# Kernel optimization log

Hardware: AMD Instinct MI355X
Metric: run time of the kernel (lower is better)

The kernel has to match this reference:

```python
import jax, jax.numpy as jnp
import numpy as np

B, S, T = 64, 512, 32
H2 = 1024          # hidden_size * 2
ATT = 512          # attention_size


def setup_inputs() -> dict:
    key = jax.random.key(0)
    k1, k2, k3, k4, k5, k6 = jax.random.split(key, 6)
    h = jax.random.normal(k1, (B, S, H2), dtype=jnp.float32)
    h_mask = jax.random.randint(k2, (B, S), 0, 2).astype(jnp.int32)
    ht = jax.random.normal(k3, (B, T, H2), dtype=jnp.float32)
    # Linear params (xavier-ish scale)
    w1_w = jax.random.normal(k4, (ATT, 2 * H2), dtype=jnp.float32) * (1.0 / np.sqrt(2 * H2))
    w1_b = jax.random.normal(k5, (ATT,), dtype=jnp.float32) * 0.02
    u_w = jax.random.normal(k6, (1, ATT), dtype=jnp.float32) * (1.0 / np.sqrt(ATT))
    return {"h": h, "h_mask": h_mask, "ht": ht, "w1_w": w1_w, "w1_b": w1_b, "u_w": u_w}


def reference(h, h_mask, ht, w1_w, w1_b, u_w):
    # h: [B,S,2H], ht: [B,T,2H], h_mask: [B,S] (1 = valid, 0 = pad)
    valid = h_mask != 0                                  # [B,S]
    ht_mean = jnp.mean(ht, axis=1, keepdims=True)        # [B,1,2H]
    h_cat = jnp.concatenate(
        [h, jnp.broadcast_to(ht_mean, h.shape)], axis=2)  # [B,S,4H]
    h_cat = jnp.where(valid[..., None], h_cat, 0.0)
    a = jnp.tanh(jnp.einsum('bsf,af->bsa', h_cat, w1_w) + w1_b)  # [B,S,ATT]
    a = jnp.where(valid[..., None], a, 0.0)
    beta = jnp.einsum('bsa,a->bs', a, u_w[0])            # [B,S]
    beta = jnp.where(valid, beta, -1e20)
    alpha = jax.nn.softmax(beta, axis=1)                 # [B,S]
    s = jnp.einsum('bs,bsd->bd', alpha, h)               # [B,2H]
    return s
```

## Files before the change

### kernel.cpp

```cpp
#include <hip/hip_runtime.h>
#include <math.h>
#include <stdint.h>

#define Bb 64
#define Ss 512
#define Tt 32
#define H2 1024
#define FF 2048
#define ATT 512
#define MM (Bb * Ss)

typedef short bf8 __attribute__((ext_vector_type(8)));
typedef float f4 __attribute__((ext_vector_type(4)));

__device__ __forceinline__ unsigned short f2bf(float f) {
    unsigned u = __float_as_uint(f);
    u = (u + 0x7fffu + ((u >> 16) & 1u)) >> 16;
    return (unsigned short)u;
}

__device__ __forceinline__ void gl_lds16(const void* g, void* l) {
    __builtin_amdgcn_global_load_lds((const __attribute__((address_space(1))) void*)g,
                                     (__attribute__((address_space(3))) void*)l, 16, 0, 0);
}

__global__ void init_kernel(float* __restrict__ beta, float* __restrict__ out) {
    int i = blockIdx.x * 256 + threadIdx.x;
    if (i < Bb * Ss) beta[i] = 0.0f;
    if (i < Bb * H2) out[i] = 0.0f;
}

__global__ void mean_kernel(const float* __restrict__ ht, float* __restrict__ ht_mean) {
    int b = blockIdx.x;
    int d4 = threadIdx.x;
    const float4* p = (const float4*)(ht + (size_t)b * Tt * H2);
    float4 acc = make_float4(0.f, 0.f, 0.f, 0.f);
    #pragma unroll 4
    for (int t = 0; t < Tt; ++t) {
        float4 v = p[(size_t)t * (H2 / 4) + d4];
        acc.x += v.x; acc.y += v.y; acc.z += v.z; acc.w += v.w;
    }
    const float inv = 1.0f / (float)Tt;
    acc.x *= inv; acc.y *= inv; acc.z *= inv; acc.w *= inv;
    ((float4*)(ht_mean + (size_t)b * H2))[d4] = acc;
}

__global__ __launch_bounds__(256) void c2_kernel2(const float* __restrict__ ht_mean,
                                                  const float* __restrict__ w1_w,
                                                  const float* __restrict__ w1_b,
                                                  float* __restrict__ c2) {
    __shared__ float hm[H2];
    int b = blockIdx.x;
    for (int i = threadIdx.x; i < H2; i += 256) hm[i] = ht_mean[(size_t)b * H2 + i];
    __syncthreads();
    int a = blockIdx.y * 64 + ((int)threadIdx.x >> 2);
    int q = (int)threadIdx.x & 3;
    const float4* w   = (const float4*)(w1_w + (size_t)a * FF + H2 + q * 256);
    const float4* hm4 = (const float4*)(hm + q * 256);
    float acc = 0.f;
    #pragma unroll 8
    for (int k = 0; k < 64; ++k) {
        float4 wv = w[k]; float4 hv = hm4[k];
        acc += wv.x * hv.x + wv.y * hv.y + wv.z * hv.z + wv.w * hv.w;
    }
    acc += __shfl_xor(acc, 1);
    acc += __shfl_xor(acc, 2);
    if (q == 0) c2[(size_t)b * ATT + a] = acc + w1_b[a];
}

__global__ void convh_kernel(const float* __restrict__ in, unsigned short* __restrict__ out) {
    size_t i = ((size_t)blockIdx.x * 256 + threadIdx.x) * 8;
    float4 a = *(const float4*)(in + i);
    float4 b = *(const float4*)(in + i + 4);
    bf8 v = { (short)f2bf(a.x), (short)f2bf(a.y), (short)f2bf(a.z), (short)f2bf(a.w),
              (short)f2bf(b.x), (short)f2bf(b.y), (short)f2bf(b.z), (short)f2bf(b.w) };
    *(bf8*)(out + i) = v;
}

__global__ void convw_kernel(const float* __restrict__ w1_w, unsigned short* __restrict__ out) {
    size_t e = ((size_t)blockIdx.x * 256 + threadIdx.x) * 8;
    int row = (int)(e >> 10);
    int c = (int)(e & 1023);
    const float* src = w1_w + (size_t)row * FF + c;
    float4 a = *(const float4*)(src);
    float4 b = *(const float4*)(src + 4);
    bf8 v = { (short)f2bf(a.x), (short)f2bf(a.y), (short)f2bf(a.z), (short)f2bf(a.w),
              (short)f2bf(b.x), (short)f2bf(b.y), (short)f2bf(b.z), (short)f2bf(b.w) };
    *(bf8*)(out + e) = v;
}

__global__ __launch_bounds__(256) void gemm_mfma_kernel(
        const unsigned short* __restrict__ hb, const unsigned short* __restrict__ wb,
        const float* __restrict__ c2, const float* __restrict__ u_w,
        float* __restrict__ beta) {
    __shared__ __align__(16) unsigned short As[128][32];
    __shared__ __align__(16) unsigned short Bs[128][32];

    const int tid = (int)threadIdx.x;
    const int m0 = blockIdx.x * 128;
    const int n0 = blockIdx.y * 128;
    const int wid = tid >> 6, lane = tid & 63;
    const int wr = (wid >> 1) * 64;
    const int wc = (wid & 1) * 64;
    const int col = lane & 15, rg = lane >> 4;

    f4 acc[4][4] = {};

    const int srow = tid >> 2;
    const int skq = (tid & 3) * 8;
    const unsigned short* a0 = hb + (size_t)(m0 + srow) * H2 + skq;
    const unsigned short* b0 = wb + (size_t)(n0 + srow) * H2 + skq;
    unsigned short* lA = &As[0][0] + (size_t)wid * 512;
    unsigned short* lB = &Bs[0][0] + (size_t)wid * 512;

    for (int k0 = 0; k0 < H2; k0 += 32) {
        gl_lds16(a0 + k0, lA);
        gl_lds16(a0 + k0 + (size_t)64 * H2, lA + 2048);
        gl_lds16(b0 + k0, lB);
        gl_lds16(b0 + k0 + (size_t)64 * H2, lB + 2048);
        __syncthreads();
        bf8 av[4], bv[4];
        #pragma unroll
        for (int i = 0; i < 4; ++i) {
            av[i] = *(const bf8*)&As[wr + i * 16 + col][rg * 8];
            bv[i] = *(const bf8*)&Bs[wc + i * 16 + col][rg * 8];
        }
        #pragma unroll
        for (int i = 0; i < 4; ++i)
            #pragma unroll
            for (int j = 0; j < 4; ++j)
                acc[i][j] = __builtin_amdgcn_mfma_f32_16x16x32_bf16(av[i], bv[j], acc[i][j], 0, 0, 0);
        __syncthreads();
    }

    const int b_idx = blockIdx.x >> 2;
    const float* c2b = c2 + (size_t)b_idx * ATT + n0 + wc;
    const float* ub = u_w + n0 + wc;
    #pragma unroll
    for (int i = 0; i < 4; ++i) {
        float rp[4] = {0.f, 0.f, 0.f, 0.f};
        #pragma unroll
        for (int j = 0; j < 4; ++j) {
            int n = j * 16 + col;
            float cv = c2b[n];
            float uv = ub[n];
            #pragma unroll
            for (int r = 0; r < 4; ++r)
                rp[r] += tanhf(acc[i][j][r] + cv) * uv;
        }
        #pragma unroll
        for (int r = 0; r < 4; ++r) {
            float v = rp[r];
            v += __shfl_xor(v, 1);
            v += __shfl_xor(v, 2);
            v += __shfl_xor(v, 4);
            v += __shfl_xor(v, 8);
            if (col == 0)
                atomicAdd(&beta[(size_t)m0 + wr + i * 16 + rg * 4 + r], v);
        }
    }
}

__global__ __launch_bounds__(256) void gemm_beta_kernel(
        const float* __restrict__ h, const float* __restrict__ w1_w,
        const float* __restrict__ c2, const float* __restrict__ u_w,
        float* __restrict__ beta) {
    __shared__ float As[32][128];
    __shared__ float Bs[32][128];
    const int m0 = blockIdx.x * 128;
    const int n0 = blockIdx.y * 128;
    const int tid = (int)threadIdx.x;
    const int lrow = tid & 31;
    const int kq = tid >> 5;
    const int tx = tid & 15;
    const int ty = tid >> 4;
    float acc[8][8] = {};
    const float* Ag = h + (size_t)(m0 + lrow) * H2 + kq * 4;
    const float* Bg = w1_w + (size_t)(n0 + lrow) * FF + kq * 4;
    for (int k0 = 0; k0 < H2; k0 += 32) {
        #pragma unroll
        for (int p = 0; p < 4; ++p) {
            float4 av = *(const float4*)(Ag + (size_t)(p * 32) * H2 + k0);
            float4 bv = *(const float4*)(Bg + (size_t)(p * 32) * FF + k0);
            int r = lrow + p * 32;
            int kk = kq * 4;
            As[kk + 0][r] = av.x; As[kk + 1][r] = av.y; As[kk + 2][r] = av.z; As[kk + 3][r] = av.w;
            Bs[kk + 0][r] = bv.x; Bs[kk + 1][r] = bv.y; Bs[kk + 2][r] = bv.z; Bs[kk + 3][r] = bv.w;
        }
        __syncthreads();
        #pragma unroll
        for (int k = 0; k < 32; ++k) {
            float4 a0 = *(const float4*)&As[k][ty * 8];
            float4 a1 = *(const float4*)&As[k][ty * 8 + 4];
            float4 b0 = *(const float4*)&Bs[k][tx * 8];
            float4 b1 = *(const float4*)&Bs[k][tx * 8 + 4];
            float av[8] = {a0.x, a0.y, a0.z, a0.w, a1.x, a1.y, a1.z, a1.w};
            float bv[8] = {b0.x, b0.y, b0.z, b0.w, b1.x, b1.y, b1.z, b1.w};
            #pragma unroll
            for (int i = 0; i < 8; ++i)
                #pragma unroll
                for (int j = 0; j < 8; ++j)
                    acc[i][j] = fmaf(av[i], bv[j], acc[i][j]);
        }
        __syncthreads();
    }
    const int b_idx = m0 / Ss;
    float rowp[8] = {};
    #pragma unroll
    for (int j = 0; j < 8; ++j) {
        int n = n0 + tx * 8 + j;
        float c2v = c2[(size_t)b_idx * ATT + n];
        float uv = u_w[n];
        #pragma unroll
        for (int i = 0; i < 8; ++i)
            rowp[i] = fmaf(tanhf(acc[i][j] + c2v), uv, rowp[i]);
    }
    #pragma unroll
    for (int i = 0; i < 8; ++i) {
        float v = rowp[i];
        v += __shfl_xor(v, 8, 16);
        v += __shfl_xor(v, 4, 16);
        v += __shfl_xor(v, 2, 16);
        v += __shfl_xor(v, 1, 16);
        if (tx == 0) atomicAdd(&beta[(size_t)m0 + ty * 8 + i], v);
    }
}

__global__ void softmax_kernel(const float* __restrict__ beta, const int* __restrict__ h_mask,
                               float* __restrict__ alpha) {
    __shared__ float red[16];
    int b = blockIdx.x;
    int s = (int)threadIdx.x;
    float v = (h_mask[(size_t)b * Ss + s] != 0) ? beta[(size_t)b * Ss + s] : -1e20f;
    float m = v;
    #pragma unroll
    for (int off = 32; off >= 1; off >>= 1) m = fmaxf(m, __shfl_xor(m, off, 64));
    int wave = s >> 6;
    if ((s & 63) == 0) red[wave] = m;
    __syncthreads();
    float mx = red[0];
    #pragma unroll
    for (int w = 1; w < 8; ++w) mx = fmaxf(mx, red[w]);
    float e = expf(v - mx);
    float sum = e;
    #pragma unroll
    for (int off = 32; off >= 1; off >>= 1) sum += __shfl_xor(sum, off, 64);
    __syncthreads();
    if ((s & 63) == 0) red[8 + wave] = sum;
    __syncthreads();
    float tot = 0.f;
    #pragma unroll
    for (int w = 0; w < 8; ++w) tot += red[8 + w];
    alpha[(size_t)b * Ss + s] = e / tot;
}

__global__ void wsum_kernel(const float* __restrict__ h, const float* __restrict__ alpha,
                            float* __restrict__ out) {
    int b = blockIdx.x;
    int d = blockIdx.y * 256 + (int)threadIdx.x;
    int s0 = blockIdx.z * 128;
    const float* hp = h + (size_t)b * Ss * H2 + (size_t)s0 * H2 + d;
    const float* ap = alpha + (size_t)b * Ss + s0;
    float acc = 0.f;
    #pragma unroll 4
    for (int s = 0; s < 128; ++s) acc = fmaf(ap[s], hp[(size_t)s * H2], acc);
    atomicAdd(&out[(size_t)b * H2 + d], acc);
}

extern "C" void kernel_launch(void* const* d_in, const int* in_sizes, int n_in,
                              void* d_out, int out_size, void* d_ws, size_t ws_size,
                              hipStream_t stream) {
    const float* h      = (const float*)d_in[0];
    const int*   h_mask = (const int*)d_in[1];
    const float* ht     = (const float*)d_in[2];
    const float* w1_w   = (const float*)d_in[3];
    const float* w1_b   = (const float*)d_in[4];
    const float* u_w    = (const float*)d_in[5];
    float* out = (float*)d_out;

    float* ws      = (float*)d_ws;
    float* ht_mean = ws;
    float* c2      = ws + 65536;
    float* beta    = ws + 98304;
    float* alpha   = ws + 131072;
    unsigned short* w1a_bf = (unsigned short*)((char*)d_ws + 659456);
    unsigned short* h_bf   = (unsigned short*)((char*)d_ws + 659456 + 1048576);
    const size_t need = 659456 + 1048576 + (size_t)MM * H2 * 2;

    hipLaunchKernelGGL(init_kernel, dim3(256), dim3(256), 0, stream, beta, out);
    hipLaunchKernelGGL(mean_kernel, dim3(Bb), dim3(256), 0, stream, ht, ht_mean);
    hipLaunchKernelGGL(c2_kernel2, dim3(Bb, 8), dim3(256), 0, stream, ht_mean, w1_w, w1_b, c2);

    if (ws_size >= need) {
        hipLaunchKernelGGL(convw_kernel, dim3(256), dim3(256), 0, stream, w1_w, w1a_bf);
        hipLaunchKernelGGL(convh_kernel, dim3(16384), dim3(256), 0, stream, h, h_bf);
        hipLaunchKernelGGL(gemm_mfma_kernel, dim3(MM / 128, ATT / 128), dim3(256), 0, stream,
                           h_bf, w1a_bf, c2, u_w, beta);
    } else {
        hipLaunchKernelGGL(gemm_beta_kernel, dim3(MM / 128, ATT / 128), dim3(256), 0, stream,
                           h, w1_w, c2, u_w, beta);
    }

    hipLaunchKernelGGL(softmax_kernel, dim3(Bb), dim3(512), 0, stream, beta, h_mask, alpha);
    hipLaunchKernelGGL(wsum_kernel, dim3(Bb, H2 / 256, 4), dim3(256), 0, stream, h, alpha, out);
}
```

Baseline: 323.2 us.

## Fuse h bf16 conversion into GEMM with full-N tiles and drop beta atomics

Removes the separate h-to-bf16 conversion pass by loading fp32 h directly in the GEMM and converting it in registers before storing to LDS. The tile changes to 64 rows by the full 512 attention columns, so each block computes complete beta rows and reduces across waves in shared memory instead of using atomics. This also removes the beta zero-init. It cuts roughly 200MB of intermediate bf16 traffic, but h loads are now plain synchronous global loads with no async LDS path, and the weight tile is re-read by 512 blocks.

```diff
diff --git a/kernel.cpp b/kernel.cpp
--- a/kernel.cpp
+++ b/kernel.cpp
@@ -10,7 +10,12 @@
 #define ATT 512
 #define MM (Bb * Ss)
 
+#define BM 64
+#define BN 512
+#define BK 32
+
 typedef short bf8 __attribute__((ext_vector_type(8)));
+typedef short bf4 __attribute__((ext_vector_type(4)));
 typedef float f4 __attribute__((ext_vector_type(4)));
 
 __device__ __forceinline__ unsigned short f2bf(float f) {
@@ -24,10 +29,9 @@
                                      (__attribute__((address_space(3))) void*)l, 16, 0, 0);
 }
 
-__global__ void init_kernel(float* __restrict__ beta, float* __restrict__ out) {
+__global__ void init_kernel(float* __restrict__ out) {
     int i = blockIdx.x * 256 + threadIdx.x;
-    if (i < Bb * Ss) beta[i] = 0.0f;
-    if (i < Bb * H2) out[i] = 0.0f;
+    out[i] = 0.0f;
 }
 
 __global__ void mean_kernel(const float* __restrict__ ht, float* __restrict__ ht_mean) {
@@ -66,15 +70,6 @@
     acc += __shfl_xor(acc, 1);
     acc += __shfl_xor(acc, 2);
     if (q == 0) c2[(size_t)b * ATT + a] = acc + w1_b[a];
-}
-
-__global__ void convh_kernel(const float* __restrict__ in, unsigned short* __restrict__ out) {
-    size_t i = ((size_t)blockIdx.x * 256 + threadIdx.x) * 8;
-    float4 a = *(const float4*)(in + i);
-    float4 b = *(const float4*)(in + i + 4);
-    bf8 v = { (short)f2bf(a.x), (short)f2bf(a.y), (short)f2bf(a.z), (short)f2bf(a.w),
-              (short)f2bf(b.x), (short)f2bf(b.y), (short)f2bf(b.z), (short)f2bf(b.w) };
-    *(bf8*)(out + i) = v;
 }
 
 __global__ void convw_kernel(const float* __restrict__ w1_w, unsigned short* __restrict__ out) {
@@ -89,41 +84,41 @@
     *(bf8*)(out + e) = v;
 }
 
-__global__ __launch_bounds__(256) void gemm_mfma_kernel(
-        const unsigned short* __restrict__ hb, const unsigned short* __restrict__ wb,
+__global__ __launch_bounds__(512) void gemm_fused_kernel(
+        const float* __restrict__ h, const unsigned short* __restrict__ wb,
         const float* __restrict__ c2, const float* __restrict__ u_w,
         float* __restrict__ beta) {
-    __shared__ __align__(16) unsigned short As[128][32];
-    __shared__ __align__(16) unsigned short Bs[128][32];
+    __shared__ __align__(16) unsigned short As[BM][BK];
+    __shared__ __align__(16) unsigned short Bs[BN][BK];
+    __shared__ float red[8][64];
 
     const int tid = (int)threadIdx.x;
-    const int m0 = blockIdx.x * 128;
-    const int n0 = blockIdx.y * 128;
+    const int m0 = blockIdx.x * BM;
     const int wid = tid >> 6, lane = tid & 63;
-    const int wr = (wid >> 1) * 64;
-    const int wc = (wid & 1) * 64;
     const int col = lane & 15, rg = lane >> 4;
 
     f4 acc[4][4] = {};
 
-    const int srow = tid >> 2;
-    const int skq = (tid & 3) * 8;
-    const unsigned short* a0 = hb + (size_t)(m0 + srow) * H2 + skq;
-    const unsigned short* b0 = wb + (size_t)(n0 + srow) * H2 + skq;
-    unsigned short* lA = &As[0][0] + (size_t)wid * 512;
+    const int arow = tid >> 3;
+    const int aq   = (tid & 7) * 4;
+    const float* Ag = h + (size_t)(m0 + arow) * H2 + aq;
+    const int brow = tid >> 2;
+    const int bq   = (tid & 3) * 8;
     unsigned short* lB = &Bs[0][0] + (size_t)wid * 512;
 
-    for (int k0 = 0; k0 < H2; k0 += 32) {
-        gl_lds16(a0 + k0, lA);
-        gl_lds16(a0 + k0 + (size_t)64 * H2, lA + 2048);
-        gl_lds16(b0 + k0, lB);
-        gl_lds16(b0 + k0 + (size_t)64 * H2, lB + 2048);
+    for (int k0 = 0; k0 < H2; k0 += BK) {
+        #pragma unroll
+        for (int c = 0; c < 4; ++c)
+            gl_lds16(wb + (size_t)(c * 128 + brow) * H2 + k0 + bq, lB + c * 4096);
+        float4 a4 = *(const float4*)(Ag + k0);
+        bf4 ab = { (short)f2bf(a4.x), (short)f2bf(a4.y), (short)f2bf(a4.z), (short)f2bf(a4.w) };
+        *(bf4*)&As[arow][aq] = ab;
         __syncthreads();
         bf8 av[4], bv[4];
         #pragma unroll
         for (int i = 0; i < 4; ++i) {
-            av[i] = *(const bf8*)&As[wr + i * 16 + col][rg * 8];
-            bv[i] = *(const bf8*)&Bs[wc + i * 16 + col][rg * 8];
+            av[i] = *(const bf8*)&As[i * 16 + col][rg * 8];
+            bv[i] = *(const bf8*)&Bs[wid * 64 + i * 16 + col][rg * 8];
         }
         #pragma unroll
         for (int i = 0; i < 4; ++i)
@@ -133,96 +128,38 @@
         __syncthreads();
     }
 
-    const int b_idx = blockIdx.x >> 2;
-    const float* c2b = c2 + (size_t)b_idx * ATT + n0 + wc;
-    const float* ub = u_w + n0 + wc;
-    #pragma unroll
-    for (int i = 0; i < 4; ++i) {
-        float rp[4] = {0.f, 0.f, 0.f, 0.f};
-        #pragma unroll
-        for (int j = 0; j < 4; ++j) {
-            int n = j * 16 + col;
-            float cv = c2b[n];
-            float uv = ub[n];
+    const int b_idx = blockIdx.x >> 3;
+    const float* c2b = c2 + (size_t)b_idx * ATT + wid * 64;
+    const float* ub  = u_w + wid * 64;
+    float rp[4][4] = {};
+    #pragma unroll
+    for (int j = 0; j < 4; ++j) {
+        int n = j * 16 + col;
+        float cv = c2b[n];
+        float uv = ub[n];
+        #pragma unroll
+        for (int i = 0; i < 4; ++i)
             #pragma unroll
             for (int r = 0; r < 4; ++r)
-                rp[r] += tanhf(acc[i][j][r] + cv) * uv;
-        }
+                rp[i][r] += tanhf(acc[i][j][r] + cv) * uv;
+    }
+    #pragma unroll
+    for (int i = 0; i < 4; ++i)
         #pragma unroll
         for (int r = 0; r < 4; ++r) {
-            float v = rp[r];
+            float v = rp[i][r];
             v += __shfl_xor(v, 1);
             v += __shfl_xor(v, 2);
             v += __shfl_xor(v, 4);
             v += __shfl_xor(v, 8);
-            if (col == 0)
-                atomicAdd(&beta[(size_t)m0 + wr + i * 16 + rg * 4 + r], v);
+            if (col == 0) red[wid][i * 16 + rg * 4 + r] = v;
         }
-    }
-}
-
-__global__ __launch_bounds__(256) void gemm_beta_kernel(
-        const float* __restrict__ h, const float* __restrict__ w1_w,
-        const float* __restrict__ c2, const float* __restrict__ u_w,
-        float* __restrict__ beta) {
-    __shared__ float As[32][128];
-    __shared__ float Bs[32][128];
-    const int m0 = blockIdx.x * 128;
-    const int n0 = blockIdx.y * 128;
-    const int tid = (int)threadIdx.x;
-    const int lrow = tid & 31;
-    const int kq = tid >> 5;
-    const int tx = tid & 15;
-    const int ty = tid >> 4;
-    float acc[8][8] = {};
-    const float* Ag = h + (size_t)(m0 + lrow) * H2 + kq * 4;
-    const float* Bg = w1_w + (size_t)(n0 + lrow) * FF + kq * 4;
-    for (int k0 = 0; k0 < H2; k0 += 32) {
-        #pragma unroll
-        for (int p = 0; p < 4; ++p) {
-            float4 av = *(const float4*)(Ag + (size_t)(p * 32) * H2 + k0);
-            float4 bv = *(const float4*)(Bg + (size_t)(p * 32) * FF + k0);
-            int r = lrow + p * 32;
-            int kk = kq * 4;
-            As[kk + 0][r] = av.x; As[kk + 1][r] = av.y; As[kk + 2][r] = av.z; As[kk + 3][r] = av.w;
-            Bs[kk + 0][r] = bv.x; Bs[kk + 1][r] = bv.y; Bs[kk + 2][r] = bv.z; Bs[kk + 3][r] = bv.w;
-        }
-        __syncthreads();
-        #pragma unroll
-        for (int k = 0; k < 32; ++k) {
-            float4 a0 = *(const float4*)&As[k][ty * 8];
-            float4 a1 = *(const float4*)&As[k][ty * 8 + 4];
-            float4 b0 = *(const float4*)&Bs[k][tx * 8];
-            float4 b1 = *(const float4*)&Bs[k][tx * 8 + 4];
-            float av[8] = {a0.x, a0.y, a0.z, a0.w, a1.x, a1.y, a1.z, a1.w};
-            float bv[8] = {b0.x, b0.y, b0.z, b0.w, b1.x, b1.y, b1.z, b1.w};
-            #pragma unroll
-            for (int i = 0; i < 8; ++i)
-                #pragma unroll
-                for (int j = 0; j < 8; ++j)
-                    acc[i][j] = fmaf(av[i], bv[j], acc[i][j]);
-        }
-        __syncthreads();
-    }
-    const int b_idx = m0 / Ss;
-    float rowp[8] = {};
-    #pragma unroll
-    for (int j = 0; j < 8; ++j) {
-        int n = n0 + tx * 8 + j;
-        float c2v = c2[(size_t)b_idx * ATT + n];
-        float uv = u_w[n];
-        #pragma unroll
-        for (int i = 0; i < 8; ++i)
-            rowp[i] = fmaf(tanhf(acc[i][j] + c2v), uv, rowp[i]);
-    }
-    #pragma unroll
-    for (int i = 0; i < 8; ++i) {
-        float v = rowp[i];
-        v += __shfl_xor(v, 8, 16);
-        v += __shfl_xor(v, 4, 16);
-        v += __shfl_xor(v, 2, 16);
-        v += __shfl_xor(v, 1, 16);
-        if (tx == 0) atomicAdd(&beta[(size_t)m0 + ty * 8 + i], v);
+    __syncthreads();
+    if (tid < 64) {
+        float s = 0.f;
+        #pragma unroll
+        for (int w = 0; w < 8; ++w) s += red[w][tid];
+        beta[(size_t)m0 + tid] = s;
     }
 }
 
@@ -283,24 +220,14 @@
     float* c2      = ws + 65536;
     float* beta    = ws + 98304;
     float* alpha   = ws + 131072;
-    unsigned short* w1a_bf = (unsigned short*)((char*)d_ws + 659456);
-    unsigned short* h_bf   = (unsigned short*)((char*)d_ws + 659456 + 1048576);
-    const size_t need = 659456 + 1048576 + (size_t)MM * H2 * 2;
-
-    hipLaunchKernelGGL(init_kernel, dim3(256), dim3(256), 0, stream, beta, out);
+    unsigned short* w1a_bf = (unsigned short*)(ws + 164864);
+
+    hipLaunchKernelGGL(init_kernel, dim3(Bb * H2 / 256), dim3(256), 0, stream, out);
     hipLaunchKernelGGL(mean_kernel, dim3(Bb), dim3(256), 0, stream, ht, ht_mean);
     hipLaunchKernelGGL(c2_kernel2, dim3(Bb, 8), dim3(256), 0, stream, ht_mean, w1_w, w1_b, c2);
-
-    if (ws_size >= need) {
-        hipLaunchKernelGGL(convw_kernel, dim3(256), dim3(256), 0, stream, w1_w, w1a_bf);
-        hipLaunchKernelGGL(convh_kernel, dim3(16384), dim3(256), 0, stream, h, h_bf);
-        hipLaunchKernelGGL(gemm_mfma_kernel, dim3(MM / 128, ATT / 128), dim3(256), 0, stream,
-                           h_bf, w1a_bf, c2, u_w, beta);
-    } else {
-        hipLaunchKernelGGL(gemm_beta_kernel, dim3(MM / 128, ATT / 128), dim3(256), 0, stream,
-                           h, w1_w, c2, u_w, beta);
-    }
-
+    hipLaunchKernelGGL(convw_kernel, dim3(256), dim3(256), 0, stream, w1_w, w1a_bf);
+    hipLaunchKernelGGL(gemm_fused_kernel, dim3(MM / BM), dim3(512), 0, stream,
+                       h, w1a_bf, c2, u_w, beta);
     hipLaunchKernelGGL(softmax_kernel, dim3(Bb), dim3(512), 0, stream, beta, h_mask, alpha);
     hipLaunchKernelGGL(wsum_kernel, dim3(Bb, H2 / 256, 4), dim3(256), 0, stream, h, alpha, out);
 }
```

After: 341.2 us. 5.6% more time.
